# Optimization experiments

Hardware: AMD Instinct MI355X
Metric: run time of the kernel (lower is better)

The kernel has to match this reference:

```python
import jax, jax.numpy as jnp
import numpy as np

B, C, H, W = 2, 64, 128, 240
DG = 8            # deformable groups
KH = KW = 3
K = KH * KW
PAD = 1
OFFSET_DIM = DG * 2 * K   # 144
MASK_DIM = DG * 1 * K     # 72


def conv2d(x, w, b):
    # x: [B,Cin,H,W], w: [Cout,Cin,kh,kw] -> [B,Cout,H,W], stride 1, pad 1
    y = jax.lax.conv_general_dilated(x, w, (1, 1), [(PAD, PAD), (PAD, PAD)],
                                     dimension_numbers=("NCHW", "OIHW", "NCHW"))
    return y + b[None, :, None, None]


def leaky_relu(x):
    return jnp.where(x >= 0, x, 0.1 * x)


def modulated_deform_conv(x, offset, mask, w, b):
    # x: [B,C,H,W]; offset: [B, DG*2*K, H, W]; mask: [B, DG*K, H, W] (already sigmoid-ed)
    # Convention: offset.reshape(B, DG, 2, K, H, W) -> [.. ,0,..]=dy, [..,1,..]=dx.
    Bx, Cx, Hx, Wx = x.shape
    cpg = Cx // DG
    ky = jnp.repeat(jnp.arange(KH) - PAD, KW).astype(x.dtype)   # [K]
    kx = jnp.tile(jnp.arange(KW) - PAD, KH).astype(x.dtype)     # [K]
    off = offset.reshape(Bx, DG, 2, K, Hx, Wx)
    hh = jnp.arange(Hx, dtype=x.dtype)
    ww = jnp.arange(Wx, dtype=x.dtype)
    py = off[:, :, 0] + hh[None, None, None, :, None] + ky[None, None, :, None, None]  # [B,DG,K,H,W]
    px = off[:, :, 1] + ww[None, None, None, None, :] + kx[None, None, :, None, None]
    y0 = jnp.floor(py)
    x0 = jnp.floor(px)
    wy = (py - y0).reshape(Bx, DG, 1, K, Hx * Wx)
    wx = (px - x0).reshape(Bx, DG, 1, K, Hx * Wx)
    y0i = y0.astype(jnp.int32)
    x0i = x0.astype(jnp.int32)
    xg = x.reshape(Bx, DG, cpg, Hx * Wx)

    def corner(yi, xi):
        valid = ((yi >= 0) & (yi < Hx) & (xi >= 0) & (xi < Wx)).astype(x.dtype)
        idx = (jnp.clip(yi, 0, Hx - 1) * Wx + jnp.clip(xi, 0, Wx - 1)).reshape(Bx, DG, K, Hx * Wx)
        gather = lambda xf, ix: xf[:, ix]                     # [cpg,K,HW]
        vals = jax.vmap(jax.vmap(gather))(xg, idx)            # [B,DG,cpg,K,HW]
        return vals * valid.reshape(Bx, DG, 1, K, Hx * Wx)

    v00 = corner(y0i, x0i)
    v01 = corner(y0i, x0i + 1)
    v10 = corner(y0i + 1, x0i)
    v11 = corner(y0i + 1, x0i + 1)
    sampled = (v00 * (1 - wy) * (1 - wx) + v01 * (1 - wy) * wx
               + v10 * wy * (1 - wx) + v11 * wy * wx)          # [B,DG,cpg,K,HW]
    sampled = sampled * mask.reshape(Bx, DG, 1, K, Hx * Wx)
    wr = w.reshape(w.shape[0], DG, cpg, K)
    out = jnp.einsum("ogck,bgckp->bop", wr, sampled).reshape(Bx, -1, Hx, Wx)
    return out + b[None, :, None, None]


def setup_inputs() -> dict:
    key = jax.random.key(0)
    ks = jax.random.split(key, 8)
    omd = OFFSET_DIM + MASK_DIM  # 216
    return {
        "nbr_fea": jax.random.normal(ks[0], (B, C, H, W), dtype=jnp.float32),
        "ref_fea": jax.random.normal(ks[1], (B, C, H, W), dtype=jnp.float32),
        # offset1_module_1: ConvReLU(2C -> C)
        "w1": 0.1 * jax.random.normal(ks[2], (C, 2 * C, 3, 3), dtype=jnp.float32),
        "b1": jnp.zeros((C,), dtype=jnp.float32),
        # offset1_module_2: Conv(C -> 216)
        "w2": 0.1 * jax.random.normal(ks[3], (omd, C, 3, 3), dtype=jnp.float32),
        "b2": jnp.zeros((omd,), dtype=jnp.float32),
        # modulated deform conv weight (C -> C)
        "wd": 0.1 * jax.random.normal(ks[4], (C, C, 3, 3), dtype=jnp.float32),
        "bd": jnp.zeros((C,), dtype=jnp.float32),
    }


def reference(nbr_fea, ref_fea, w1, b1, w2, b2, wd, bd):
    fea = jnp.concatenate([nbr_fea, ref_fea], axis=1)          # [B,2C,H,W]
    h = leaky_relu(conv2d(fea, w1, b1))                        # [B,C,H,W]
    offset_mask = conv2d(h, w2, b2)                            # [B,216,H,W]
    o1, o2, m = jnp.split(offset_mask, 3, axis=1)              # 72 each
    offset_curr = jnp.concatenate([o1, o2], axis=1)            # [B,144,H,W]
    mask = jax.nn.sigmoid(m)                                   # [B,72,H,W]
    aligned = modulated_deform_conv(nbr_fea, offset_curr, mask, wd, bd)
    return aligned, offset_curr
```

## Files before the change

### kernel.cpp

```cpp
#include <hip/hip_runtime.h>
#include <cstdint>
#include <cmath>

#define B_ 2
#define C_ 64
#define H_ 128
#define W_ 240
#define HW_ (H_*W_)
#define OFF_CH 144
#define MASK_CH 72
#define ALIGNED_SZ (B_*C_*HW_)

typedef __bf16 bf16x8 __attribute__((ext_vector_type(8)));
typedef float f32x4 __attribute__((ext_vector_type(4)));
typedef short short4v __attribute__((ext_vector_type(4)));
typedef unsigned short ushort_t;

__device__ __forceinline__ ushort_t f2bf(float f) {
    unsigned u = __float_as_uint(f);
    u += 0x7fffu + ((u >> 16) & 1u);
    return (ushort_t)(u >> 16);
}
__device__ __forceinline__ float bf2f(ushort_t b) {
    return __uint_as_float((unsigned)b << 16);
}
__device__ __forceinline__ float bf_lo(int q) {
    return __uint_as_float((unsigned)q << 16);
}
__device__ __forceinline__ float bf_hi(int q) {
    return __uint_as_float((unsigned)q & 0xffff0000u);
}

#define W1P_OFF  0u
#define W2P_OFF  147456u
#define PIN_OFF  442368u
#define HBUF_OFF 16171008u
#define MASK_OFF 24035328u
#define WDP_OFF  32882688u

__global__ __launch_bounds__(256) void pack_weights(
    const float* __restrict__ w1, const float* __restrict__ w2,
    const float* __restrict__ wd,
    ushort_t* __restrict__ w1pf, ushort_t* __restrict__ w2pf,
    ushort_t* __restrict__ wdp)
{
    int t = blockIdx.x * 256 + threadIdx.x;
    if (t < 73728) {
        int j = t & 7, lane = (t >> 3) & 63, r = t >> 9;
        int wv = r & 3, ct = r >> 2;
        int tap = ct % 9, chunk = ct / 9;
        int oc = wv * 16 + (lane & 15);
        int ci = chunk * 32 + ((lane >> 4) << 3) + j;
        w1pf[t] = f2bf(w1[((size_t)oc * 128 + ci) * 9 + tap]);
    } else if (t < 73728 + 147456) {
        int f = t - 73728;
        int j = f & 7, lane = (f >> 3) & 63, r = f >> 9;
        int wv = r & 3, q = r >> 2;
        int tap = q % 9, oc2 = q / 9;
        int chunk = oc2 & 1, ocg = oc2 >> 1;
        int oc = ocg * 64 + wv * 16 + (lane & 15);
        int ci = chunk * 32 + ((lane >> 4) << 3) + j;
        float v = (oc < 216) ? w2[((size_t)oc * 64 + ci) * 9 + tap] : 0.f;
        w2pf[f] = f2bf(v);
    } else if (t < 73728 + 147456 + 36864) {
        int f = t - 221184;
        int j = f & 7, lane = (f >> 3) & 63, sg = f >> 9;
        int g = sg & 3, s = sg >> 2;
        int oc = g * 16 + (lane & 15);
        int K = s * 32 + ((lane >> 4) << 3) + j;
        int dg = K / 72, rr = K - dg * 72;
        int tap = rr >> 3, ci = (dg << 3) + (rr & 7);
        wdp[f] = f2bf(wd[((size_t)oc * 64 + ci) * 9 + tap]);
    }
}

__global__ __launch_bounds__(256) void pack_input(
    const float* __restrict__ nbr, const float* __restrict__ ref,
    ushort_t* __restrict__ pin)
{
    int f = blockIdx.x * 256 + threadIdx.x;
    int civec = f & 15;
    int rem = f >> 4;
    int b = rem / HW_, pix = rem - b * HW_;
    const int half = civec >> 3;
    const float* src = (half == 0) ? (nbr + (size_t)b * 64 * HW_)
                                   : (ref + (size_t)b * 64 * HW_);
    int cbase = (civec & 7) * 8;
    union { ushort_t u[8]; int4 v; } o;
#pragma unroll
    for (int j = 0; j < 8; ++j)
        o.u[j] = f2bf(src[(size_t)(cbase + j) * HW_ + pix]);
    *(int4*)&pin[(((size_t)b * 2 + half) * HW_ + pix) * 64 + cbase] = o.v;
}

__global__ __launch_bounds__(256) void conv1_mfma(
    const ushort_t* __restrict__ pin, const float* __restrict__ b1,
    const ushort_t* __restrict__ w1pf, ushort_t* __restrict__ hbuf)
{
    const int bx = blockIdx.x, y = blockIdx.y, b = blockIdx.z;
    const int x0 = bx * 48;
    const int tid = threadIdx.x;
    const int wv = tid >> 6, lane = tid & 63;
    const int l15 = lane & 15, k8 = (lane >> 4) << 3;

    __shared__ __align__(16) ushort_t s_in[3 * 50 * 40];

    f32x4 acc[3];
#pragma unroll
    for (int i = 0; i < 3; ++i) acc[i] = (f32x4){0.f, 0.f, 0.f, 0.f};

    for (int chunk = 0; chunk < 4; ++chunk) {
        const int ci0 = chunk << 5;
        for (int i = tid; i < 600; i += 256) {
            int cvec = i & 3, rc = i >> 2;
            int row = rc / 50, col = rc - row * 50;
            int gy = y + row - 1, gx = x0 + col - 1;
            int ci = ci0 + cvec * 8;
            int half = ci >> 6, cw = ci & 63;
            int4 v = {0, 0, 0, 0};
            if ((unsigned)gy < (unsigned)H_ && (unsigned)gx < (unsigned)W_)
                v = *(const int4*)&pin[(((size_t)b * 2 + half) * HW_ + (size_t)gy * W_ + gx) * 64 + cw];
            *(int4*)&s_in[(row * 50 + col) * 40 + cvec * 8] = v;
        }
        bf16x8 af[9];
#pragma unroll
        for (int tap = 0; tap < 9; ++tap)
            af[tap] = *(const bf16x8*)&w1pf[((((size_t)chunk * 9 + tap) * 4 + wv) * 64 + lane) * 8];
        __syncthreads();

#pragma unroll
        for (int tap = 0; tap < 9; ++tap) {
            const int ky = tap / 3, kx = tap - ky * 3;
#pragma unroll
            for (int pt = 0; pt < 3; ++pt) {
                int col = (pt << 4) + l15 + kx;
                bf16x8 bb = *(const bf16x8*)&s_in[(ky * 50 + col) * 40 + k8];
                acc[pt] = __builtin_amdgcn_mfma_f32_16x16x32_bf16(af[tap], bb, acc[pt], 0, 0, 0);
            }
        }
        __syncthreads();
    }

    const int ocb = (wv << 4) + ((lane >> 4) << 2);
    float bias[4];
#pragma unroll
    for (int r = 0; r < 4; ++r) bias[r] = b1[ocb + r];
#pragma unroll
    for (int pt = 0; pt < 3; ++pt) {
        int gx = x0 + (pt << 4) + l15;
        union { ushort_t u[4]; short4v s; } o;
#pragma unroll
        for (int r = 0; r < 4; ++r) {
            float v = acc[pt][r] + bias[r];
            v = (v >= 0.f) ? v : 0.1f * v;
            o.u[r] = f2bf(v);
        }
        *(short4v*)&hbuf[(((size_t)b * H_ + y) * W_ + gx) * 64 + ocb] = o.s;
    }
}

__global__ __launch_bounds__(256) void conv2_mfma(
    const ushort_t* __restrict__ hbuf, const float* __restrict__ b2,
    const ushort_t* __restrict__ w2pf,
    float* __restrict__ off_out, ushort_t* __restrict__ maskbuf)
{
    const int bx = blockIdx.x, y = blockIdx.y;
    const int b = blockIdx.z >> 2, ocg = blockIdx.z & 3;
    const int x0 = bx * 48;
    const int tid = threadIdx.x;
    const int wv = tid >> 6, lane = tid & 63;
    const int l15 = lane & 15, k8 = (lane >> 4) << 3;

    __shared__ __align__(16) ushort_t s_in[3 * 50 * 40];

    f32x4 acc[3];
#pragma unroll
    for (int i = 0; i < 3; ++i) acc[i] = (f32x4){0.f, 0.f, 0.f, 0.f};

    for (int chunk = 0; chunk < 2; ++chunk) {
        const int ci0 = chunk << 5;
        for (int i = tid; i < 600; i += 256) {
            int cvec = i & 3, rc = i >> 2;
            int row = rc / 50, col = rc - row * 50;
            int gy = y + row - 1, gx = x0 + col - 1;
            int4 v = {0, 0, 0, 0};
            if ((unsigned)gy < (unsigned)H_ && (unsigned)gx < (unsigned)W_)
                v = *(const int4*)&hbuf[(((size_t)b * H_ + gy) * W_ + gx) * 64 + ci0 + cvec * 8];
            *(int4*)&s_in[(row * 50 + col) * 40 + cvec * 8] = v;
        }
        bf16x8 af[9];
#pragma unroll
        for (int tap = 0; tap < 9; ++tap)
            af[tap] = *(const bf16x8*)&w2pf[(((((size_t)ocg * 2 + chunk) * 9 + tap) * 4 + wv) * 64 + lane) * 8];
        __syncthreads();

#pragma unroll
        for (int tap = 0; tap < 9; ++tap) {
            const int ky = tap / 3, kx = tap - ky * 3;
#pragma unroll
            for (int pt = 0; pt < 3; ++pt) {
                int col = (pt << 4) + l15 + kx;
                bf16x8 bb = *(const bf16x8*)&s_in[(ky * 50 + col) * 40 + k8];
                acc[pt] = __builtin_amdgcn_mfma_f32_16x16x32_bf16(af[tap], bb, acc[pt], 0, 0, 0);
            }
        }
        __syncthreads();
    }

    const int ocb = (wv << 4) + ((lane >> 4) << 2);
#pragma unroll
    for (int pt = 0; pt < 3; ++pt) {
        int gx = x0 + (pt << 4) + l15;
#pragma unroll
        for (int r = 0; r < 4; ++r) {
            int co = (ocg << 6) + ocb + r;
            if (co < 216) {
                float v = acc[pt][r] + b2[co];
                if (co < 144) {
                    off_out[((size_t)b * OFF_CH + co) * HW_ + y * W_ + gx] = v;
                } else {
                    maskbuf[((size_t)b * MASK_CH + (co - 144)) * HW_ + y * W_ + gx] =
                        f2bf(1.f / (1.f + expf(-v)));
                }
            }
        }
    }
}

__global__ __launch_bounds__(256) void dconv_mfma(
    const ushort_t* __restrict__ pin,
    const float* __restrict__ offs,
    const ushort_t* __restrict__ maskbuf,
    const ushort_t* __restrict__ wdp, const float* __restrict__ bd,
    float* __restrict__ outp)
{
    const int bid = blockIdx.x;
    const int nid = (bid & 7) * 60 + (bid >> 3);
    const int b   = nid / 240;
    const int rr_ = nid - b * 240;
    const int byt = rr_ / 15, bxt = rr_ - byt * 15;
    const int x0 = bxt << 4, y0 = byt << 3;

    const int tid = threadIdx.x;
    const int wv = tid >> 6, lane = tid & 63;
    const int l15 = lane & 15, hi4 = lane >> 4;

    const size_t pinb = ((size_t)b * 2) * HW_;

    __shared__ __align__(16) ushort_t s_S[128 * 40];

    f32x4 acc[8];
#pragma unroll
    for (int i = 0; i < 8; ++i) acc[i] = (f32x4){0.f, 0.f, 0.f, 0.f};

    for (int s = 0; s < 18; ++s) {
#pragma unroll
        for (int half = 0; half < 2; ++half) {
            const int t = tid + half * 256;
            const int pxl = t & 127;
            const int g = t >> 7;
            const int row = pxl >> 4, col = pxl & 15;
            const int x = x0 + col, y = y0 + row;
            const size_t pix = (size_t)y * W_ + x;

            const int Kb = (s << 5) + (g << 3);
            const int dg = Kb / 72;
            const int rr = Kb - dg * 72;
            const int tap = rr >> 3;
            const int ky = tap / 3 - 1, kx = tap % 3 - 1;

            float dyv = offs[((size_t)b * OFF_CH + dg * 18 + tap) * HW_ + pix];
            float dxv = offs[((size_t)b * OFF_CH + dg * 18 + 9 + tap) * HW_ + pix];
            float m   = bf2f(maskbuf[((size_t)b * MASK_CH + dg * 9 + tap) * HW_ + pix]);

            float py  = (float)(y + ky) + dyv;
            float pxf = (float)(x + kx) + dxv;
            float yf = floorf(py), xf = floorf(pxf);
            float wy = py - yf, wx = pxf - xf;
            int yi = (int)yf, xi = (int)xf;

            const bool y0v = (unsigned)yi < (unsigned)H_;
            const bool y1v = (unsigned)(yi + 1) < (unsigned)H_;
            const bool x0v = (unsigned)xi < (unsigned)W_;
            const bool x1v = (unsigned)(xi + 1) < (unsigned)W_;

            float w00 = (1.f - wy) * (1.f - wx) * m; if (!(y0v && x0v)) w00 = 0.f;
            float w01 = (1.f - wy) * wx        * m; if (!(y0v && x1v)) w01 = 0.f;
            float w10 = wy        * (1.f - wx) * m; if (!(y1v && x0v)) w10 = 0.f;
            float w11 = wy        * wx         * m; if (!(y1v && x1v)) w11 = 0.f;

            int yc0 = min(max(yi, 0), H_ - 1), yc1 = min(max(yi + 1, 0), H_ - 1);
            int xc0 = min(max(xi, 0), W_ - 1), xc1 = min(max(xi + 1, 0), W_ - 1);

            const int cofs = dg << 3;
            int4 q00 = *(const int4*)&pin[(pinb + yc0 * W_ + xc0) * 64 + cofs];
            int4 q01 = *(const int4*)&pin[(pinb + yc0 * W_ + xc1) * 64 + cofs];
            int4 q10 = *(const int4*)&pin[(pinb + yc1 * W_ + xc0) * 64 + cofs];
            int4 q11 = *(const int4*)&pin[(pinb + yc1 * W_ + xc1) * 64 + cofs];

            union { ushort_t u[8]; int4 v; } o;
            const int* a00 = (const int*)&q00; const int* a01 = (const int*)&q01;
            const int* a10 = (const int*)&q10; const int* a11 = (const int*)&q11;
#pragma unroll
            for (int j = 0; j < 4; ++j) {
                float lo = w00 * bf_lo(a00[j]) + w01 * bf_lo(a01[j])
                         + w10 * bf_lo(a10[j]) + w11 * bf_lo(a11[j]);
                float hv = w00 * bf_hi(a00[j]) + w01 * bf_hi(a01[j])
                         + w10 * bf_hi(a10[j]) + w11 * bf_hi(a11[j]);
                o.u[2 * j]     = f2bf(lo);
                o.u[2 * j + 1] = f2bf(hv);
            }
            *(int4*)&s_S[pxl * 40 + (g << 3)] = o.v;
        }
        __syncthreads();

        bf16x8 a = *(const bf16x8*)&wdp[(((size_t)(s << 2) + wv) * 64 + lane) << 3];
#pragma unroll
        for (int pg = 0; pg < 8; ++pg) {
            bf16x8 bb = *(const bf16x8*)&s_S[((pg << 4) + l15) * 40 + (hi4 << 3)];
            acc[pg] = __builtin_amdgcn_mfma_f32_16x16x32_bf16(a, bb, acc[pg], 0, 0, 0);
        }
        __syncthreads();
    }

    const int ocb = (wv << 4) + (hi4 << 2);
#pragma unroll
    for (int pg = 0; pg < 8; ++pg) {
#pragma unroll
        for (int r = 0; r < 4; ++r) {
            int oc = ocb + r;
            outp[((size_t)b * C_ + oc) * HW_ + (size_t)(y0 + pg) * W_ + x0 + l15] =
                acc[pg][r] + bd[oc];
        }
    }
}

extern "C" void kernel_launch(void* const* d_in, const int* in_sizes, int n_in,
                              void* d_out, int out_size, void* d_ws, size_t ws_size,
                              hipStream_t stream)
{
    const float* nbr = (const float*)d_in[0];
    const float* ref = (const float*)d_in[1];
    const float* w1  = (const float*)d_in[2];
    const float* b1  = (const float*)d_in[3];
    const float* w2  = (const float*)d_in[4];
    const float* b2  = (const float*)d_in[5];
    const float* wd  = (const float*)d_in[6];
    const float* bd  = (const float*)d_in[7];

    float* out     = (float*)d_out;
    float* off_out = out + ALIGNED_SZ;

    char* ws = (char*)d_ws;
    ushort_t* w1pf  = (ushort_t*)(ws + W1P_OFF);
    ushort_t* w2pf  = (ushort_t*)(ws + W2P_OFF);
    ushort_t* pin   = (ushort_t*)(ws + PIN_OFF);
    ushort_t* hbufp = (ushort_t*)(ws + HBUF_OFF);
    ushort_t* maskp = (ushort_t*)(ws + MASK_OFF);
    ushort_t* wdp   = (ushort_t*)(ws + WDP_OFF);

    dim3 blk(256, 1, 1);
    pack_weights<<<1008, blk, 0, stream>>>(w1, w2, wd, w1pf, w2pf, wdp);
    pack_input<<<3840, blk, 0, stream>>>(nbr, ref, pin);
    conv1_mfma<<<dim3(5, 128, 2), blk, 0, stream>>>(pin, b1, w1pf, hbufp);
    conv2_mfma<<<dim3(5, 128, 8), blk, 0, stream>>>(hbufp, b2, w2pf, off_out, maskp);
    dconv_mfma<<<480, blk, 0, stream>>>(pin, off_out, maskp, wdp, bd, out);
}
```

Before: 150.6 us.

## Software-pipeline deformable sampling with double-buffered LDS and smaller tiles

Restructures the deformable conv kernel so each thread samples one pixel per stage. The bilinear gathers for stage s+1 are issued before the MFMA work of stage s, using a double-buffered shared-memory tile so only one barrier per stage is needed. The tile shrinks from 16x8 to 16x4 pixels and the grid doubles to 960 blocks, which gives more parallelism. The cost is extra registers for the prefetched data, and the weight fragment is now reused across fewer MFMAs.

```diff
diff --git a/kernel.cpp b/kernel.cpp
--- a/kernel.cpp
+++ b/kernel.cpp
@@ -235,97 +235,121 @@
     float* __restrict__ outp)
 {
     const int bid = blockIdx.x;
-    const int nid = (bid & 7) * 60 + (bid >> 3);
-    const int b   = nid / 240;
-    const int rr_ = nid - b * 240;
+    const int nid = (bid & 7) * 120 + (bid >> 3);
+    const int b   = nid / 480;
+    const int rr_ = nid - b * 480;
     const int byt = rr_ / 15, bxt = rr_ - byt * 15;
-    const int x0 = bxt << 4, y0 = byt << 3;
+    const int x0 = bxt << 4, y0 = byt << 2;
 
     const int tid = threadIdx.x;
     const int wv = tid >> 6, lane = tid & 63;
     const int l15 = lane & 15, hi4 = lane >> 4;
 
-    const size_t pinb = ((size_t)b * 2) * HW_;
-
-    __shared__ __align__(16) ushort_t s_S[128 * 40];
-
-    f32x4 acc[8];
-#pragma unroll
-    for (int i = 0; i < 8; ++i) acc[i] = (f32x4){0.f, 0.f, 0.f, 0.f};
-
+    const int x = x0 + l15, y = y0 + hi4;
+    const size_t pix = (size_t)y * W_ + x;
+    const size_t pinb = (size_t)(b * 2) * HW_;
+    const size_t offb = (size_t)b * OFF_CH * HW_ + pix;
+    const size_t mskb = (size_t)b * MASK_CH * HW_ + pix;
+
+    __shared__ __align__(16) ushort_t s_S[2][64 * 40];
+
+    f32x4 acc[4];
+#pragma unroll
+    for (int i = 0; i < 4; ++i) acc[i] = (f32x4){0.f, 0.f, 0.f, 0.f};
+
+    float cw0, cw1, cw2, cw3;
+    int4 q0, q1, q2, q3;
+
+    auto sample_issue = [&](int dg, int tap, float dyv, float dxv, float m,
+                            float& w00, float& w01, float& w10, float& w11,
+                            int4& r00, int4& r01, int4& r10, int4& r11) {
+        const int ky = tap / 3 - 1, kx = tap % 3 - 1;
+        float py  = (float)(y + ky) + dyv;
+        float pxf = (float)(x + kx) + dxv;
+        float yf = floorf(py), xf = floorf(pxf);
+        float wy = py - yf, wx = pxf - xf;
+        int yi = (int)yf, xi = (int)xf;
+        const bool y0v = (unsigned)yi < (unsigned)H_;
+        const bool y1v = (unsigned)(yi + 1) < (unsigned)H_;
+        const bool x0v = (unsigned)xi < (unsigned)W_;
+        const bool x1v = (unsigned)(xi + 1) < (unsigned)W_;
+        w00 = (1.f - wy) * (1.f - wx) * m; if (!(y0v && x0v)) w00 = 0.f;
+        w01 = (1.f - wy) * wx        * m; if (!(y0v && x1v)) w01 = 0.f;
+        w10 = wy        * (1.f - wx) * m; if (!(y1v && x0v)) w10 = 0.f;
+        w11 = wy        * wx         * m; if (!(y1v && x1v)) w11 = 0.f;
+        int yc0 = min(max(yi, 0), H_ - 1), yc1 = min(max(yi + 1, 0), H_ - 1);
+        int xc0 = min(max(xi, 0), W_ - 1), xc1 = min(max(xi + 1, 0), W_ - 1);
+        const int cofs = dg << 3;
+        r00 = *(const int4*)&pin[(pinb + yc0 * W_ + xc0) * 64 + cofs];
+        r01 = *(const int4*)&pin[(pinb + yc0 * W_ + xc1) * 64 + cofs];
+        r10 = *(const int4*)&pin[(pinb + yc1 * W_ + xc0) * 64 + cofs];
+        r11 = *(const int4*)&pin[(pinb + yc1 * W_ + xc1) * 64 + cofs];
+    };
+
+    {
+        const int Kb = (wv << 3);
+        const int dg = Kb / 72, rr = Kb - dg * 72, tap = rr >> 3;
+        float dyv = offs[offb + (size_t)(dg * 18 + tap) * HW_];
+        float dxv = offs[offb + (size_t)(dg * 18 + 9 + tap) * HW_];
+        float m   = bf2f(maskbuf[mskb + (size_t)(dg * 9 + tap) * HW_]);
+        sample_issue(dg, tap, dyv, dxv, m, cw0, cw1, cw2, cw3, q0, q1, q2, q3);
+    }
+
+    int c = 0;
+#pragma unroll
     for (int s = 0; s < 18; ++s) {
-#pragma unroll
-        for (int half = 0; half < 2; ++half) {
-            const int t = tid + half * 256;
-            const int pxl = t & 127;
-            const int g = t >> 7;
-            const int row = pxl >> 4, col = pxl & 15;
-            const int x = x0 + col, y = y0 + row;
-            const size_t pix = (size_t)y * W_ + x;
-
-            const int Kb = (s << 5) + (g << 3);
-            const int dg = Kb / 72;
-            const int rr = Kb - dg * 72;
-            const int tap = rr >> 3;
-            const int ky = tap / 3 - 1, kx = tap % 3 - 1;
-
-            float dyv = offs[((size_t)b * OFF_CH + dg * 18 + tap) * HW_ + pix];
-            float dxv = offs[((size_t)b * OFF_CH + dg * 18 + 9 + tap) * HW_ + pix];
-            float m   = bf2f(maskbuf[((size_t)b * MASK_CH + dg * 9 + tap) * HW_ + pix]);
-
-            float py  = (float)(y + ky) + dyv;
-            float pxf = (float)(x + kx) + dxv;
-            float yf = floorf(py), xf = floorf(pxf);
-            float wy = py - yf, wx = pxf - xf;
-            int yi = (int)yf, xi = (int)xf;
-
-            const bool y0v = (unsigned)yi < (unsigned)H_;
-            const bool y1v = (unsigned)(yi + 1) < (unsigned)H_;
-            const bool x0v = (unsigned)xi < (unsigned)W_;
-            const bool x1v = (unsigned)(xi + 1) < (unsigned)W_;
-
-            float w00 = (1.f - wy) * (1.f - wx) * m; if (!(y0v && x0v)) w00 = 0.f;
-            float w01 = (1.f - wy) * wx        * m; if (!(y0v && x1v)) w01 = 0.f;
-            float w10 = wy        * (1.f - wx) * m; if (!(y1v && x0v)) w10 = 0.f;
-            float w11 = wy        * wx         * m; if (!(y1v && x1v)) w11 = 0.f;
-
-            int yc0 = min(max(yi, 0), H_ - 1), yc1 = min(max(yi + 1, 0), H_ - 1);
-            int xc0 = min(max(xi, 0), W_ - 1), xc1 = min(max(xi + 1, 0), W_ - 1);
-
-            const int cofs = dg << 3;
-            int4 q00 = *(const int4*)&pin[(pinb + yc0 * W_ + xc0) * 64 + cofs];
-            int4 q01 = *(const int4*)&pin[(pinb + yc0 * W_ + xc1) * 64 + cofs];
-            int4 q10 = *(const int4*)&pin[(pinb + yc1 * W_ + xc0) * 64 + cofs];
-            int4 q11 = *(const int4*)&pin[(pinb + yc1 * W_ + xc1) * 64 + cofs];
-
+        float dyn = 0.f, dxn = 0.f, mn = 0.f;
+        int dgN = 0, tapN = 0;
+        if (s < 17) {
+            const int Kb = ((s + 1) << 5) + (wv << 3);
+            dgN = Kb / 72;
+            const int rr = Kb - dgN * 72;
+            tapN = rr >> 3;
+            dyn = offs[offb + (size_t)(dgN * 18 + tapN) * HW_];
+            dxn = offs[offb + (size_t)(dgN * 18 + 9 + tapN) * HW_];
+            mn  = bf2f(maskbuf[mskb + (size_t)(dgN * 9 + tapN) * HW_]);
+        }
+        bf16x8 afrag = *(const bf16x8*)&wdp[(((size_t)(s << 2) + wv) * 64 + lane) << 3];
+
+        {
             union { ushort_t u[8]; int4 v; } o;
-            const int* a00 = (const int*)&q00; const int* a01 = (const int*)&q01;
-            const int* a10 = (const int*)&q10; const int* a11 = (const int*)&q11;
+            const int* a00 = (const int*)&q0; const int* a01 = (const int*)&q1;
+            const int* a10 = (const int*)&q2; const int* a11 = (const int*)&q3;
 #pragma unroll
             for (int j = 0; j < 4; ++j) {
-                float lo = w00 * bf_lo(a00[j]) + w01 * bf_lo(a01[j])
-                         + w10 * bf_lo(a10[j]) + w11 * bf_lo(a11[j]);
-                float hv = w00 * bf_hi(a00[j]) + w01 * bf_hi(a01[j])
-                         + w10 * bf_hi(a10[j]) + w11 * bf_hi(a11[j]);
+                float lo = cw0 * bf_lo(a00[j]) + cw1 * bf_lo(a01[j])
+                         + cw2 * bf_lo(a10[j]) + cw3 * bf_lo(a11[j]);
+                float hv = cw0 * bf_hi(a00[j]) + cw1 * bf_hi(a01[j])
+                         + cw2 * bf_hi(a10[j]) + cw3 * bf_hi(a11[j]);
                 o.u[2 * j]     = f2bf(lo);
                 o.u[2 * j + 1] = f2bf(hv);
             }
-            *(int4*)&s_S[pxl * 40 + (g << 3)] = o.v;
-        }
-        __syncthreads();
-
-        bf16x8 a = *(const bf16x8*)&wdp[(((size_t)(s << 2) + wv) * 64 + lane) << 3];
-#pragma unroll
-        for (int pg = 0; pg < 8; ++pg) {
-            bf16x8 bb = *(const bf16x8*)&s_S[((pg << 4) + l15) * 40 + (hi4 << 3)];
-            acc[pg] = __builtin_amdgcn_mfma_f32_16x16x32_bf16(a, bb, acc[pg], 0, 0, 0);
-        }
-        __syncthreads();
+            *(int4*)&s_S[c][lane * 40 + (wv << 3)] = o.v;
+        }
+
+        float nw0, nw1, nw2, nw3;
+        int4 n0, n1, n2, n3;
+        if (s < 17)
+            sample_issue(dgN, tapN, dyn, dxn, mn, nw0, nw1, nw2, nw3, n0, n1, n2, n3);
+
+        __syncthreads();
+
+#pragma unroll
+        for (int pg = 0; pg < 4; ++pg) {
+            bf16x8 bb = *(const bf16x8*)&s_S[c][((pg << 4) + l15) * 40 + (hi4 << 3)];
+            acc[pg] = __builtin_amdgcn_mfma_f32_16x16x32_bf16(afrag, bb, acc[pg], 0, 0, 0);
+        }
+
+        c ^= 1;
+        if (s < 17) {
+            cw0 = nw0; cw1 = nw1; cw2 = nw2; cw3 = nw3;
+            q0 = n0; q1 = n1; q2 = n2; q3 = n3;
+        }
     }
 
     const int ocb = (wv << 4) + (hi4 << 2);
 #pragma unroll
-    for (int pg = 0; pg < 8; ++pg) {
+    for (int pg = 0; pg < 4; ++pg) {
 #pragma unroll
         for (int r = 0; r < 4; ++r) {
             int oc = ocb + r;
@@ -364,5 +388,5 @@
     pack_input<<<3840, blk, 0, stream>>>(nbr, ref, pin);
     conv1_mfma<<<dim3(5, 128, 2), blk, 0, stream>>>(pin, b1, w1pf, hbufp);
     conv2_mfma<<<dim3(5, 128, 8), blk, 0, stream>>>(hbufp, b2, w2pf, off_out, maskp);
-    dconv_mfma<<<480, blk, 0, stream>>>(pin, off_out, maskp, wdp, bd, out);
-}
+    dconv_mfma<<<960, blk, 0, stream>>>(pin, off_out, maskp, wdp, bd, out);
+}
```

Result: faster. 146.4 us (-2.8%).

## Restructure deform conv to register-direct MFMA operands with software-pipelined sampling

Applied to the files above, without the earlier changes.

The deformable conv kernel no longer stages bilinear samples through shared memory with two barriers per K-step. Each wave now samples its own pixel row straight into the MFMA B-fragment and computes all 64 output channels using four accumulators. Offset loads are prefetched two steps ahead and corner gathers one step ahead to hide gather latency. Tiles shrink to 16x4, the grid doubles to 960 blocks, and launch bounds ask for 4 blocks per CU. In exchange, each wave loads the weight fragments itself and register pressure goes up.

```diff
diff --git a/kernel.cpp b/kernel.cpp
--- a/kernel.cpp
+++ b/kernel.cpp
@@ -227,7 +227,7 @@
     }
 }
 
-__global__ __launch_bounds__(256) void dconv_mfma(
+__global__ __launch_bounds__(256, 4) void dconv_mfma(
     const ushort_t* __restrict__ pin,
     const float* __restrict__ offs,
     const ushort_t* __restrict__ maskbuf,
@@ -235,103 +235,117 @@
     float* __restrict__ outp)
 {
     const int bid = blockIdx.x;
-    const int nid = (bid & 7) * 60 + (bid >> 3);
-    const int b   = nid / 240;
-    const int rr_ = nid - b * 240;
+    const int nid = (bid & 7) * 120 + (bid >> 3);
+    const int b   = nid / 480;
+    const int rr_ = nid - b * 480;
     const int byt = rr_ / 15, bxt = rr_ - byt * 15;
-    const int x0 = bxt << 4, y0 = byt << 3;
+    const int x0 = bxt << 4, y0 = byt << 2;
 
     const int tid = threadIdx.x;
     const int wv = tid >> 6, lane = tid & 63;
     const int l15 = lane & 15, hi4 = lane >> 4;
 
-    const size_t pinb = ((size_t)b * 2) * HW_;
-
-    __shared__ __align__(16) ushort_t s_S[128 * 40];
-
-    f32x4 acc[8];
-#pragma unroll
-    for (int i = 0; i < 8; ++i) acc[i] = (f32x4){0.f, 0.f, 0.f, 0.f};
-
+    const int x = x0 + l15, y = y0 + wv;
+    const size_t pix = (size_t)y * W_ + x;
+    const size_t pinb = (size_t)(b * 2) * HW_;
+    const float* offp = offs + (size_t)b * OFF_CH * HW_ + pix;
+    const ushort_t* mkp = maskbuf + (size_t)b * MASK_CH * HW_ + pix;
+
+    f32x4 acc0 = {0.f,0.f,0.f,0.f}, acc1 = {0.f,0.f,0.f,0.f};
+    f32x4 acc2 = {0.f,0.f,0.f,0.f}, acc3 = {0.f,0.f,0.f,0.f};
+
+    auto load_off = [&](int s, float& dy, float& dx, float& m) {
+        int K = (s << 5) + (hi4 << 3);
+        int dg = K / 72, r2 = K - dg * 72, tap = r2 >> 3;
+        dy = offp[(size_t)(dg * 18 + tap) * HW_];
+        dx = offp[(size_t)(dg * 18 + 9 + tap) * HW_];
+        m  = bf2f(mkp[(size_t)(dg * 9 + tap) * HW_]);
+    };
+    auto sample = [&](int s, float dyv, float dxv, float m,
+                      float& r0, float& r1, float& r2, float& r3,
+                      int4& g0, int4& g1, int4& g2, int4& g3) {
+        int K = (s << 5) + (hi4 << 3);
+        int dg = K / 72, rm = K - dg * 72, tap = rm >> 3;
+        int ky = tap / 3 - 1, kx = tap % 3 - 1;
+        float py  = (float)(y + ky) + dyv;
+        float pxf = (float)(x + kx) + dxv;
+        float yf = floorf(py), xf = floorf(pxf);
+        float wy = py - yf, wx = pxf - xf;
+        int yi = (int)yf, xi = (int)xf;
+        bool y0v = (unsigned)yi < (unsigned)H_;
+        bool y1v = (unsigned)(yi + 1) < (unsigned)H_;
+        bool x0v = (unsigned)xi < (unsigned)W_;
+        bool x1v = (unsigned)(xi + 1) < (unsigned)W_;
+        r0 = (1.f - wy) * (1.f - wx) * m; if (!(y0v && x0v)) r0 = 0.f;
+        r1 = (1.f - wy) * wx         * m; if (!(y0v && x1v)) r1 = 0.f;
+        r2 = wy         * (1.f - wx) * m; if (!(y1v && x0v)) r2 = 0.f;
+        r3 = wy         * wx         * m; if (!(y1v && x1v)) r3 = 0.f;
+        int yc0 = min(max(yi, 0), H_ - 1), yc1 = min(max(yi + 1, 0), H_ - 1);
+        int xc0 = min(max(xi, 0), W_ - 1), xc1 = min(max(xi + 1, 0), W_ - 1);
+        const int cofs = dg << 3;
+        g0 = *(const int4*)&pin[(pinb + yc0 * W_ + xc0) * 64 + cofs];
+        g1 = *(const int4*)&pin[(pinb + yc0 * W_ + xc1) * 64 + cofs];
+        g2 = *(const int4*)&pin[(pinb + yc1 * W_ + xc0) * 64 + cofs];
+        g3 = *(const int4*)&pin[(pinb + yc1 * W_ + xc1) * 64 + cofs];
+    };
+
+    float dyA, dxA, mA;
+    float w0, w1, w2, w3;
+    int4 q0, q1, q2, q3;
+    load_off(0, dyA, dxA, mA);
+    sample(0, dyA, dxA, mA, w0, w1, w2, w3, q0, q1, q2, q3);
+    load_off(1, dyA, dxA, mA);
+
+#pragma unroll 2
     for (int s = 0; s < 18; ++s) {
-#pragma unroll
-        for (int half = 0; half < 2; ++half) {
-            const int t = tid + half * 256;
-            const int pxl = t & 127;
-            const int g = t >> 7;
-            const int row = pxl >> 4, col = pxl & 15;
-            const int x = x0 + col, y = y0 + row;
-            const size_t pix = (size_t)y * W_ + x;
-
-            const int Kb = (s << 5) + (g << 3);
-            const int dg = Kb / 72;
-            const int rr = Kb - dg * 72;
-            const int tap = rr >> 3;
-            const int ky = tap / 3 - 1, kx = tap % 3 - 1;
-
-            float dyv = offs[((size_t)b * OFF_CH + dg * 18 + tap) * HW_ + pix];
-            float dxv = offs[((size_t)b * OFF_CH + dg * 18 + 9 + tap) * HW_ + pix];
-            float m   = bf2f(maskbuf[((size_t)b * MASK_CH + dg * 9 + tap) * HW_ + pix]);
-
-            float py  = (float)(y + ky) + dyv;
-            float pxf = (float)(x + kx) + dxv;
-            float yf = floorf(py), xf = floorf(pxf);
-            float wy = py - yf, wx = pxf - xf;
-            int yi = (int)yf, xi = (int)xf;
-
-            const bool y0v = (unsigned)yi < (unsigned)H_;
-            const bool y1v = (unsigned)(yi + 1) < (unsigned)H_;
-            const bool x0v = (unsigned)xi < (unsigned)W_;
-            const bool x1v = (unsigned)(xi + 1) < (unsigned)W_;
-
-            float w00 = (1.f - wy) * (1.f - wx) * m; if (!(y0v && x0v)) w00 = 0.f;
-            float w01 = (1.f - wy) * wx        * m; if (!(y0v && x1v)) w01 = 0.f;
-            float w10 = wy        * (1.f - wx) * m; if (!(y1v && x0v)) w10 = 0.f;
-            float w11 = wy        * wx         * m; if (!(y1v && x1v)) w11 = 0.f;
-
-            int yc0 = min(max(yi, 0), H_ - 1), yc1 = min(max(yi + 1, 0), H_ - 1);
-            int xc0 = min(max(xi, 0), W_ - 1), xc1 = min(max(xi + 1, 0), W_ - 1);
-
-            const int cofs = dg << 3;
-            int4 q00 = *(const int4*)&pin[(pinb + yc0 * W_ + xc0) * 64 + cofs];
-            int4 q01 = *(const int4*)&pin[(pinb + yc0 * W_ + xc1) * 64 + cofs];
-            int4 q10 = *(const int4*)&pin[(pinb + yc1 * W_ + xc0) * 64 + cofs];
-            int4 q11 = *(const int4*)&pin[(pinb + yc1 * W_ + xc1) * 64 + cofs];
-
-            union { ushort_t u[8]; int4 v; } o;
-            const int* a00 = (const int*)&q00; const int* a01 = (const int*)&q01;
-            const int* a10 = (const int*)&q10; const int* a11 = (const int*)&q11;
+        float dyB = 0.f, dxB = 0.f, mB = 0.f;
+        if (s + 2 < 18) load_off(s + 2, dyB, dxB, mB);
+
+        const ushort_t* wp = wdp + (((size_t)(s << 2) * 64) + lane) * 8;
+        bf16x8 a0 = *(const bf16x8*)(wp);
+        bf16x8 a1 = *(const bf16x8*)(wp + 512);
+        bf16x8 a2 = *(const bf16x8*)(wp + 1024);
+        bf16x8 a3 = *(const bf16x8*)(wp + 1536);
+
+        float nw0, nw1, nw2, nw3;
+        int4 n0, n1, n2, n3;
+        if (s + 1 < 18)
+            sample(s + 1, dyA, dxA, mA, nw0, nw1, nw2, nw3, n0, n1, n2, n3);
+
+        bf16x8 bfrag;
+        {
+            const int* c00 = (const int*)&q0; const int* c01 = (const int*)&q1;
+            const int* c10 = (const int*)&q2; const int* c11 = (const int*)&q3;
 #pragma unroll
             for (int j = 0; j < 4; ++j) {
-                float lo = w00 * bf_lo(a00[j]) + w01 * bf_lo(a01[j])
-                         + w10 * bf_lo(a10[j]) + w11 * bf_lo(a11[j]);
-                float hv = w00 * bf_hi(a00[j]) + w01 * bf_hi(a01[j])
-                         + w10 * bf_hi(a10[j]) + w11 * bf_hi(a11[j]);
-                o.u[2 * j]     = f2bf(lo);
-                o.u[2 * j + 1] = f2bf(hv);
+                float lo = w0 * bf_lo(c00[j]) + w1 * bf_lo(c01[j])
+                         + w2 * bf_lo(c10[j]) + w3 * bf_lo(c11[j]);
+                float hv = w0 * bf_hi(c00[j]) + w1 * bf_hi(c01[j])
+                         + w2 * bf_hi(c10[j]) + w3 * bf_hi(c11[j]);
+                bfrag[2 * j]     = (__bf16)lo;
+                bfrag[2 * j + 1] = (__bf16)hv;
             }
-            *(int4*)&s_S[pxl * 40 + (g << 3)] = o.v;
-        }
-        __syncthreads();
-
-        bf16x8 a = *(const bf16x8*)&wdp[(((size_t)(s << 2) + wv) * 64 + lane) << 3];
-#pragma unroll
-        for (int pg = 0; pg < 8; ++pg) {
-            bf16x8 bb = *(const bf16x8*)&s_S[((pg << 4) + l15) * 40 + (hi4 << 3)];
-            acc[pg] = __builtin_amdgcn_mfma_f32_16x16x32_bf16(a, bb, acc[pg], 0, 0, 0);
-        }
-        __syncthreads();
-    }
-
-    const int ocb = (wv << 4) + (hi4 << 2);
-#pragma unroll
-    for (int pg = 0; pg < 8; ++pg) {
-#pragma unroll
-        for (int r = 0; r < 4; ++r) {
-            int oc = ocb + r;
-            outp[((size_t)b * C_ + oc) * HW_ + (size_t)(y0 + pg) * W_ + x0 + l15] =
-                acc[pg][r] + bd[oc];
-        }
+        }
+
+        acc0 = __builtin_amdgcn_mfma_f32_16x16x32_bf16(a0, bfrag, acc0, 0, 0, 0);
+        acc1 = __builtin_amdgcn_mfma_f32_16x16x32_bf16(a1, bfrag, acc1, 0, 0, 0);
+        acc2 = __builtin_amdgcn_mfma_f32_16x16x32_bf16(a2, bfrag, acc2, 0, 0, 0);
+        acc3 = __builtin_amdgcn_mfma_f32_16x16x32_bf16(a3, bfrag, acc3, 0, 0, 0);
+
+        dyA = dyB; dxA = dxB; mA = mB;
+        w0 = nw0; w1 = nw1; w2 = nw2; w3 = nw3;
+        q0 = n0; q1 = n1; q2 = n2; q3 = n3;
+    }
+
+    const int ocr = hi4 << 2;
+    const size_t pbase = (size_t)b * C_ * HW_ + (size_t)y * W_ + x0 + l15;
+#pragma unroll
+    for (int r = 0; r < 4; ++r) {
+        int oc0 = ocr + r;
+        outp[pbase + (size_t)(oc0)      * HW_] = acc0[r] + bd[oc0];
+        outp[pbase + (size_t)(oc0 + 16) * HW_] = acc1[r] + bd[oc0 + 16];
+        outp[pbase + (size_t)(oc0 + 32) * HW_] = acc2[r] + bd[oc0 + 32];
+        outp[pbase + (size_t)(oc0 + 48) * HW_] = acc3[r] + bd[oc0 + 48];
     }
 }
 
@@ -364,5 +378,5 @@
     pack_input<<<3840, blk, 0, stream>>>(nbr, ref, pin);
     conv1_mfma<<<dim3(5, 128, 2), blk, 0, stream>>>(pin, b1, w1pf, hbufp);
     conv2_mfma<<<dim3(5, 128, 8), blk, 0, stream>>>(hbufp, b2, w2pf, off_out, maskp);
-    dconv_mfma<<<480, blk, 0, stream>>>(pin, off_out, maskp, wdp, bd, out);
-}
+    dconv_mfma<<<960, blk, 0, stream>>>(pin, off_out, maskp, wdp, bd, out);
+}
```

After: 153.3 us. No clear change (+1.8%).
